# Performance work log

Measured on AMD Instinct MI355X. Metric: run time of the kernel, lower is better.

Reference implementation:

```python
import jax, jax.numpy as jnp
import numpy as np
import math

B, S, K, H, NH = 4, 1024, 512, 1024, 16
HD = H // NH  # 64


def _split_heads(x):
    # [B, L, H] -> [B, NH, L, HD]
    b, l, _ = x.shape
    return x.reshape(b, l, NH, HD).transpose(0, 2, 1, 3)


def setup_inputs() -> dict:
    key = jax.random.key(0)
    ks = jax.random.split(key, 16)
    scale = 1.0 / math.sqrt(H)
    d = {
        'hidden_states': jax.random.normal(ks[0], (B, S, H), jnp.float32),
        'encoder_hidden_states': jax.random.normal(ks[1], (B, K, H), jnp.float32),
        'attention_mask': jnp.zeros((B, 1, 1, S), jnp.float32),
        'encoder_attention_mask': jnp.zeros((B, 1, 1, K), jnp.float32),
    }
    names = ['q', 'k', 'v', 'kq', 'kk', 'kv']
    for i, n in enumerate(names):
        d[f'W{n}'] = jax.random.normal(ks[2 + i], (H, H), jnp.float32) * scale
        d[f'b{n}'] = jnp.zeros((H,), jnp.float32)
    return d


def reference(hidden_states, encoder_hidden_states, attention_mask, encoder_attention_mask,
              Wq, bq, Wk, bk, Wv, bv, Wkq, bkq, Wkk, bkk, Wkv, bkv):
    inv = 1.0 / math.sqrt(HD)
    # self branch
    q = _split_heads(hidden_states @ Wq + bq)            # [B,NH,S,HD]
    k = _split_heads(hidden_states @ Wk + bk)
    v = _split_heads(hidden_states @ Wv + bv)
    scores = jnp.einsum('bhsd,bhtd->bhst', q, k) * inv + attention_mask
    probs = jax.nn.softmax(scores, axis=-1)              # [B,NH,S,S]
    ctx = jnp.einsum('bhst,bhtd->bhsd', probs, v)
    # knowledge branch
    kq = _split_heads(hidden_states @ Wkq + bkq)          # [B,NH,S,HD]
    kk = _split_heads(encoder_hidden_states @ Wkk + bkk)  # [B,NH,K,HD]
    kv = _split_heads(encoder_hidden_states @ Wkv + bkv)
    kscores = jnp.einsum('bhsd,bhtd->bhst', kq, kk) * inv + encoder_attention_mask
    kprobs = jax.nn.softmax(kscores, axis=-1)            # [B,NH,S,K]
    kctx = jnp.einsum('bhst,bhtd->bhsd', kprobs, kv)
    # merge heads and average branches
    out = (ctx + kctx) * 0.5                             # [B,NH,S,HD]
    out = out.transpose(0, 2, 1, 3).reshape(B, S, H)
    return out
```

## Files before the change

kernel.cpp:

```cpp
#include <hip/hip_runtime.h>

#define BATCH 4
#define SEQ   1024
#define KENC  512
#define HDIM  1024
#define NHEAD 16
#define HD    64
#define LOG2E 1.44269504088896340736f

typedef __attribute__((ext_vector_type(8))) short bf16x8;
typedef __attribute__((ext_vector_type(4))) float f32x4;
typedef __attribute__((ext_vector_type(16))) float f32x16;
typedef __attribute__((ext_vector_type(4))) float f4v;
typedef __attribute__((ext_vector_type(4))) short s4v;

__device__ __forceinline__ short f2bf(float f) {
  unsigned u = __float_as_uint(f);
  u += 0x7fffu + ((u >> 16) & 1u);
  return (short)(u >> 16);
}

__device__ __forceinline__ void gload_lds16(const void* g, void* l) {
  __builtin_amdgcn_global_load_lds(
      (const __attribute__((address_space(1))) void*)g,
      (__attribute__((address_space(3))) void*)l, 16, 0, 0);
}

__global__ __launch_bounds__(256) void cast_bf16(const float* __restrict__ src,
                                                 short* __restrict__ dst, int n4) {
  int i = blockIdx.x * 256 + threadIdx.x;
  if (i >= n4) return;
  f4v v = ((const f4v*)src)[i];
  s4v o;
#pragma unroll
  for (int j = 0; j < 4; ++j) o[j] = f2bf(v[j]);
  ((s4v*)dst)[i] = o;
}

struct WtArgs { const float* W[6]; };

__global__ __launch_bounds__(256) void wt_cast(WtArgs a, short* __restrict__ wt) {
  int j = blockIdx.z;
  const float* W = a.W[j];
  short* dst = wt + (size_t)j * (HDIM * HDIM);
  int cb = blockIdx.x * 32, rb = blockIdx.y * 32;
  __shared__ float t[32][33];
  int tx = threadIdx.x & 31, ty = threadIdx.x >> 5;
#pragma unroll
  for (int rr = 0; rr < 4; ++rr)
    t[ty + rr * 8][tx] = W[(size_t)(rb + ty + rr * 8) * HDIM + cb + tx];
  __syncthreads();
#pragma unroll
  for (int rr = 0; rr < 4; ++rr)
    dst[(size_t)(cb + ty + rr * 8) * HDIM + rb + tx] = f2bf(t[tx][ty + rr * 8]);
}

struct ProjArgs {
  const short* X[6];
  const short* Wt[6];
  const float* bias[6];
  short* out[6];
  int M[6];
  int tshift[6];
  int mode[6];
  float scale[6];
};

__global__ __launch_bounds__(256) void proj_gemm(ProjArgs a) {
  int job = blockIdx.z;
  int M = a.M[job];
  int by = blockIdx.y;
  if (by * 128 >= M) return;
  int bx = blockIdx.x;
  const short* X = a.X[job];
  const short* W = a.Wt[job];

  __shared__ short As[128 * 32];
  __shared__ short Bs[128 * 32];

  int tid = threadIdx.x, lane = tid & 63, wave = tid >> 6;
  int wr = wave >> 1, wc = wave & 1;
  int l15 = lane & 15, g4 = lane >> 4;

  f32x4 acc[4][4];
#pragma unroll
  for (int m = 0; m < 4; ++m)
#pragma unroll
    for (int n = 0; n < 4; ++n)
#pragma unroll
      for (int r = 0; r < 4; ++r) acc[m][n][r] = 0.0f;

  int arow = by * 128, brow = bx * 128;
  const int crow = lane >> 2;
  const int sgrp = (lane & 3) ^ ((lane >> 2) & 3) ^ (lane >> 4);
  const int rsw = (lane & 3) ^ ((l15) >> 2);

  for (int k0 = 0; k0 < HDIM; k0 += 32) {
#pragma unroll
    for (int cc = 0; cc < 2; ++cc) {
      int c = wave * 2 + cc;
      gload_lds16(X + (size_t)(arow + c * 16 + crow) * HDIM + k0 + sgrp * 8,
                  (char*)As + c * 1024);
      gload_lds16(W + (size_t)(brow + c * 16 + crow) * HDIM + k0 + sgrp * 8,
                  (char*)Bs + c * 1024);
    }
    __syncthreads();
    bf16x8 af[4], bfr[4];
#pragma unroll
    for (int m = 0; m < 4; ++m)
      af[m] = *(const bf16x8*)((const char*)As + (wr * 64 + m * 16 + l15) * 64 +
                               ((g4 ^ rsw) << 4));
#pragma unroll
    for (int n = 0; n < 4; ++n)
      bfr[n] = *(const bf16x8*)((const char*)Bs + (wc * 64 + n * 16 + l15) * 64 +
                                ((g4 ^ rsw) << 4));
#pragma unroll
    for (int m = 0; m < 4; ++m)
#pragma unroll
      for (int n = 0; n < 4; ++n)
        acc[m][n] = __builtin_amdgcn_mfma_f32_16x16x32_bf16(af[m], bfr[n],
                                                            acc[m][n], 0, 0, 0);
    __syncthreads();
  }

  const float* bias = a.bias[job];
  short* out = a.out[job];
  int tshift = a.tshift[job], tmask = (1 << tshift) - 1, mode = a.mode[job];
  float scl = a.scale[job];
#pragma unroll
  for (int m = 0; m < 4; ++m) {
    int rowb = arow + wr * 64 + m * 16 + (g4 << 2);
#pragma unroll
    for (int n = 0; n < 4; ++n) {
      int col = brow + wc * 64 + n * 16 + l15;
      float bv = bias[col];
      int head = col >> 6, d = col & 63;
#pragma unroll
      for (int r = 0; r < 4; ++r) {
        int row = rowb + r;
        int bb = row >> tshift, t = row & tmask;
        float val = (acc[m][n][r] + bv) * scl;
        size_t idx;
        if (mode == 0)
          idx = ((((size_t)bb * NHEAD + head) << tshift) + t) * 64 + d;
        else
          idx = ((((size_t)bb * NHEAD + head) * 64 + d) << tshift) + t;
        out[idx] = f2bf(val);
      }
    }
  }
}

__global__ __launch_bounds__(256, 3) void attn32(
    const short* __restrict__ qall, const short* __restrict__ kall,
    const short* __restrict__ vTall, const short* __restrict__ kqall,
    const short* __restrict__ kkall, const short* __restrict__ kvTall,
    const float* __restrict__ amask, const float* __restrict__ emask,
    float* __restrict__ out) {
  __shared__ char KT[2][8192];
  __shared__ char VT[2][8192];
  __shared__ float red[4][32];

  int lid = blockIdx.x;
  int id = (lid & 7) * 64 + (lid >> 3);
  int bh = id >> 3, qb = id & 7;
  int b = bh >> 4, h = bh & 15;
  int lane = threadIdx.x & 63, wave = threadIdx.x >> 6;
  int l31 = lane & 31, hi = lane >> 5, x7 = l31 & 7;
  int qrow0 = qb * 128 + wave * 32;

  bf16x8 qcur[4];
  {
    const short* qp = qall + ((size_t)bh * SEQ + qrow0 + l31) * 64;
#pragma unroll
    for (int i = 0; i < 4; ++i)
      qcur[i] = *(const bf16x8*)(qp + i * 16 + hi * 8);
  }

  const char* kb0 = (const char*)(kall + (size_t)bh * SEQ * 64);
  const char* vb0 = (const char*)(vTall + (size_t)bh * 64 * SEQ);
  const char* kb1 = (const char*)(kkall + (size_t)bh * KENC * 64);
  const char* vb1 = (const char*)(kvTall + (size_t)bh * 64 * KENC);
  const float* mpc = amask + (size_t)b * SEQ;

  auto STAGE = [&](int pb, const char* kb, const char* vb, size_t vrowb, int kt) {
    int t0 = threadIdx.x;
#pragma unroll
    for (int c = 0; c < 2; ++c) {
      int idx = c * 256 + t0;
      int row = idx >> 3, phys = idx & 7;
      int lg = phys ^ (row & 7);
      gload_lds16(kb + ((size_t)(kt * 64 + row)) * 128 + lg * 16,
                  KT[pb] + idx * 16);
      gload_lds16(vb + (size_t)row * vrowb + (size_t)kt * 128 + lg * 16,
                  VT[pb] + idx * 16);
    }
  };

  STAGE(0, kb0, vb0, SEQ * 2, 0);

  f32x16 ctx0, ctx1, c10, c11;
#pragma unroll
  for (int r = 0; r < 16; ++r) { ctx0[r] = 0.f; ctx1[r] = 0.f; c10[r] = 0.f; c11[r] = 0.f; }
  float mr = -1e30f, lr = 0.f;

#pragma unroll 1
  for (int t = 0; t < 24; ++t) {
    int p = t & 1;
    __syncthreads();
    if (t < 23) {
      int tn = t + 1;
      if (tn >= 16) STAGE(p ^ 1, kb1, vb1, KENC * 2, tn - 16);
      else          STAGE(p ^ 1, kb0, vb0, SEQ * 2, tn);
    }
    if (t == 16) {
      if (!hi) red[wave][l31] = lr;
      asm volatile("s_waitcnt lgkmcnt(0)" ::: "memory");
#pragma unroll
      for (int r2 = 0; r2 < 4; ++r2) {
        f4v lv = *(const f4v*)(&red[wave][r2 * 8 + 4 * hi]);
#pragma unroll
        for (int j2 = 0; j2 < 4; ++j2) {
          float li = __builtin_amdgcn_rcpf(lv[j2]);
          int r = r2 * 4 + j2;
          c10[r] = ctx0[r] * li;  ctx0[r] = 0.f;
          c11[r] = ctx1[r] * li;  ctx1[r] = 0.f;
        }
      }
      mr = -1e30f; lr = 0.f;
      const short* kqp = kqall + ((size_t)bh * SEQ + qrow0 + l31) * 64;
#pragma unroll
      for (int i = 0; i < 4; ++i)
        qcur[i] = *(const bf16x8*)(kqp + i * 16 + hi * 8);
      mpc = emask + (size_t)b * KENC;
    }
    int kt = (t >= 16) ? t - 16 : t;
    const char* Kp = KT[p];
    const char* Vp = VT[p];

    f32x16 s0, s1;
#pragma unroll
    for (int r = 0; r < 16; ++r) { s0[r] = 0.f; s1[r] = 0.f; }
    __builtin_amdgcn_s_setprio(1);
#pragma unroll
    for (int i = 0; i < 4; ++i) {
      bf16x8 kf = *(const bf16x8*)(Kp + (l31)*128 + (((2 * i + hi) ^ x7) << 4));
      s0 = __builtin_amdgcn_mfma_f32_32x32x16_bf16(kf, qcur[i], s0, 0, 0, 0);
    }
#pragma unroll
    for (int i = 0; i < 4; ++i) {
      bf16x8 kf = *(const bf16x8*)(Kp + (32 + l31) * 128 + (((2 * i + hi) ^ x7) << 4));
      s1 = __builtin_amdgcn_mfma_f32_32x32x16_bf16(kf, qcur[i], s1, 0, 0, 0);
    }
    __builtin_amdgcn_s_setprio(0);

    const float* mp = mpc + kt * 64;
#pragma unroll
    for (int r2 = 0; r2 < 4; ++r2) {
      f4v ma = *(const f4v*)(mp + r2 * 8 + 4 * hi);
      f4v mb = *(const f4v*)(mp + 32 + r2 * 8 + 4 * hi);
#pragma unroll
      for (int j2 = 0; j2 < 4; ++j2) {
        s0[r2 * 4 + j2] = fmaf(ma[j2], LOG2E, s0[r2 * 4 + j2]);
        s1[r2 * 4 + j2] = fmaf(mb[j2], LOG2E, s1[r2 * 4 + j2]);
      }
    }

    float mx = s0[0];
#pragma unroll
    for (int r = 1; r < 16; ++r) mx = fmaxf(mx, s0[r]);
#pragma unroll
    for (int r = 0; r < 16; ++r) mx = fmaxf(mx, s1[r]);
    mx = fmaxf(mx, __int_as_float(__shfl_xor(__float_as_int(mx), 32)));

    if (!__all(mx <= mr + 12.f)) {
      float mn = fmaxf(mr, mx);
      float scl = __builtin_amdgcn_exp2f(mr - mn);
      mr = mn; lr *= scl;
      if (!hi) red[wave][l31] = scl;
      asm volatile("s_waitcnt lgkmcnt(0)" ::: "memory");
#pragma unroll
      for (int r2 = 0; r2 < 4; ++r2) {
        f4v sv = *(const f4v*)(&red[wave][r2 * 8 + 4 * hi]);
#pragma unroll
        for (int j2 = 0; j2 < 4; ++j2) {
          ctx0[r2 * 4 + j2] *= sv[j2];
          ctx1[r2 * 4 + j2] *= sv[j2];
        }
      }
    }

    float rs = 0.f;
#pragma unroll
    for (int r = 0; r < 16; ++r) { s0[r] = __builtin_amdgcn_exp2f(s0[r] - mr); rs += s0[r]; }
#pragma unroll
    for (int r = 0; r < 16; ++r) { s1[r] = __builtin_amdgcn_exp2f(s1[r] - mr); rs += s1[r]; }
    rs += __int_as_float(__shfl_xor(__float_as_int(rs), 32));
    lr += rs;

#pragma unroll
    for (int s = 0; s < 2; ++s) {
      const f32x16& sv = s ? s1 : s0;
      unsigned W[8];
#pragma unroll
      for (int r2 = 0; r2 < 4; ++r2) {
        asm("v_cvt_pk_bf16_f32 %0, %1, %2"
            : "=v"(W[r2 * 2]) : "v"(sv[r2 * 4 + 0]), "v"(sv[r2 * 4 + 1]));
        asm("v_cvt_pk_bf16_f32 %0, %1, %2"
            : "=v"(W[r2 * 2 + 1]) : "v"(sv[r2 * 4 + 2]), "v"(sv[r2 * 4 + 3]));
      }
#pragma unroll
      for (int jr = 0; jr < 2; ++jr) {
        unsigned sendA = hi ? W[(2 * jr) * 2]     : W[(2 * jr + 1) * 2];
        unsigned sendB = hi ? W[(2 * jr) * 2 + 1] : W[(2 * jr + 1) * 2 + 1];
        unsigned rA = (unsigned)__shfl_xor((int)sendA, 32);
        unsigned rB = (unsigned)__shfl_xor((int)sendB, 32);
        union { unsigned u[4]; bf16x8 v; } pa;
        if (!hi) { pa.u[0] = W[2 * jr * 2]; pa.u[1] = W[2 * jr * 2 + 1];
                   pa.u[2] = rA;            pa.u[3] = rB; }
        else     { pa.u[0] = rA;            pa.u[1] = rB;
                   pa.u[2] = W[(2 * jr + 1) * 2]; pa.u[3] = W[(2 * jr + 1) * 2 + 1]; }
        int j = s * 2 + jr;
        __builtin_amdgcn_s_setprio(1);
        bf16x8 vf0 = *(const bf16x8*)(Vp + (l31)*128 + (((2 * j + hi) ^ x7) << 4));
        ctx0 = __builtin_amdgcn_mfma_f32_32x32x16_bf16(pa.v, vf0, ctx0, 0, 0, 0);
        bf16x8 vf1 = *(const bf16x8*)(Vp + (32 + l31) * 128 + (((2 * j + hi) ^ x7) << 4));
        ctx1 = __builtin_amdgcn_mfma_f32_32x32x16_bf16(pa.v, vf1, ctx1, 0, 0, 0);
        __builtin_amdgcn_s_setprio(0);
      }
    }
  }

  if (!hi) red[wave][l31] = lr;
  asm volatile("s_waitcnt lgkmcnt(0)" ::: "memory");
  float* op = out + ((size_t)b * SEQ) * HDIM + h * 64 + l31;
#pragma unroll
  for (int r2 = 0; r2 < 4; ++r2) {
    f4v lv = *(const f4v*)(&red[wave][r2 * 8 + 4 * hi]);
#pragma unroll
    for (int j2 = 0; j2 < 4; ++j2) {
      float li = __builtin_amdgcn_rcpf(lv[j2]);
      int s = qrow0 + r2 * 8 + 4 * hi + j2;
      int r = r2 * 4 + j2;
      op[(size_t)s * HDIM]      = 0.5f * (c10[r] + ctx0[r] * li);
      op[(size_t)s * HDIM + 32] = 0.5f * (c11[r] + ctx1[r] * li);
    }
  }
}

extern "C" void kernel_launch(void* const* d_in, const int* in_sizes, int n_in,
                              void* d_out, int out_size, void* d_ws, size_t ws_size,
                              hipStream_t stream) {
  const float* hid = (const float*)d_in[0];
  const float* enc = (const float*)d_in[1];
  const float* amask = (const float*)d_in[2];
  const float* emask = (const float*)d_in[3];

  char* ws = (char*)d_ws;
  short* hbf = (short*)(ws);
  short* ebf = (short*)(ws + (8u << 20));
  short* wt = (short*)(ws + (12u << 20));
  short* qo = (short*)(ws + (24u << 20));
  short* ko = (short*)(ws + (32u << 20));
  short* vT = (short*)(ws + (40u << 20));
  short* kqo = (short*)(ws + (48u << 20));
  short* kko = (short*)(ws + (56u << 20));
  short* kvT = (short*)(ws + (60u << 20));

  cast_bf16<<<4096, 256, 0, stream>>>(hid, hbf, (BATCH * SEQ * HDIM) / 4);
  cast_bf16<<<2048, 256, 0, stream>>>(enc, ebf, (BATCH * KENC * HDIM) / 4);

  WtArgs wa;
  for (int j = 0; j < 6; ++j) wa.W[j] = (const float*)d_in[4 + 2 * j];
  wt_cast<<<dim3(32, 32, 6), 256, 0, stream>>>(wa, wt);

  ProjArgs pa;
  const short* Xs[6] = {hbf, hbf, hbf, hbf, ebf, ebf};
  short* outs[6] = {qo, ko, vT, kqo, kko, kvT};
  const int Ms[6] = {4096, 4096, 4096, 4096, 2048, 2048};
  const int tsh[6] = {10, 10, 10, 10, 9, 9};
  const int md[6] = {0, 0, 1, 0, 0, 1};
  const float qscale = 0.125f * LOG2E;
  const float scl[6] = {qscale, 1.f, 1.f, qscale, 1.f, 1.f};
  for (int j = 0; j < 6; ++j) {
    pa.X[j] = Xs[j];
    pa.Wt[j] = wt + (size_t)j * (HDIM * HDIM);
    pa.bias[j] = (const float*)d_in[5 + 2 * j];
    pa.out[j] = outs[j];
    pa.M[j] = Ms[j];
    pa.tshift[j] = tsh[j];
    pa.mode[j] = md[j];
    pa.scale[j] = scl[j];
  }
  proj_gemm<<<dim3(8, 32, 6), 256, 0, stream>>>(pa);

  attn32<<<512, 256, 0, stream>>>(qo, ko, vT, kqo, kko, kvT, amask, emask,
                                  (float*)d_out);
}
```

Measured before the change: 147.6 us.

## Pipeline projection GEMM with four-stage LDS ring buffer and async prefetch

Replaces the single-buffered load/sync/compute loop in the projection GEMM with a four-buffer LDS ring. Three K-tiles are prefetched ahead with direct global-to-LDS loads, and partial vmcnt waits let global loads overlap the MFMA work. Wave priority is raised around the MFMA block. The cost is 64KB of LDS per block, which can lower occupancy, and more complex hand-managed waits and barriers.

```diff
diff --git a/kernel.cpp b/kernel.cpp
--- a/kernel.cpp
+++ b/kernel.cpp
@@ -75,8 +75,7 @@
   const short* X = a.X[job];
   const short* W = a.Wt[job];
 
-  __shared__ short As[128 * 32];
-  __shared__ short Bs[128 * 32];
+  __shared__ __align__(16) char Lds[4][16384];
 
   int tid = threadIdx.x, lane = tid & 63, wave = tid >> 6;
   int wr = wave >> 1, wc = wave & 1;
@@ -93,35 +92,73 @@
   int arow = by * 128, brow = bx * 128;
   const int crow = lane >> 2;
   const int sgrp = (lane & 3) ^ ((lane >> 2) & 3) ^ (lane >> 4);
-  const int rsw = (lane & 3) ^ ((l15) >> 2);
-
-  for (int k0 = 0; k0 < HDIM; k0 += 32) {
-#pragma unroll
-    for (int cc = 0; cc < 2; ++cc) {
-      int c = wave * 2 + cc;
-      gload_lds16(X + (size_t)(arow + c * 16 + crow) * HDIM + k0 + sgrp * 8,
-                  (char*)As + c * 1024);
-      gload_lds16(W + (size_t)(brow + c * 16 + crow) * HDIM + k0 + sgrp * 8,
-                  (char*)Bs + c * 1024);
-    }
-    __syncthreads();
-    bf16x8 af[4], bfr[4];
-#pragma unroll
-    for (int m = 0; m < 4; ++m)
-      af[m] = *(const bf16x8*)((const char*)As + (wr * 64 + m * 16 + l15) * 64 +
-                               ((g4 ^ rsw) << 4));
-#pragma unroll
-    for (int n = 0; n < 4; ++n)
-      bfr[n] = *(const bf16x8*)((const char*)Bs + (wc * 64 + n * 16 + l15) * 64 +
-                                ((g4 ^ rsw) << 4));
-#pragma unroll
-    for (int m = 0; m < 4; ++m)
-#pragma unroll
-      for (int n = 0; n < 4; ++n)
-        acc[m][n] = __builtin_amdgcn_mfma_f32_16x16x32_bf16(af[m], bfr[n],
-                                                            acc[m][n], 0, 0, 0);
-    __syncthreads();
-  }
+  const int rsw = (lane & 3) ^ (l15 >> 2);
+
+  const short* Xb = X + (size_t)arow * HDIM + (size_t)crow * HDIM + sgrp * 8;
+  const short* Wb = W + (size_t)brow * HDIM + (size_t)crow * HDIM + sgrp * 8;
+
+#define STAGE(buf, kt)                                                        \
+  do {                                                                        \
+    _Pragma("unroll") for (int cc = 0; cc < 2; ++cc) {                        \
+      int c = wave * 2 + cc;                                                  \
+      gload_lds16(Xb + (size_t)c * 16 * HDIM + (kt) * 32,                     \
+                  (char*)Lds[buf] + c * 1024 + lane * 16);                    \
+      gload_lds16(Wb + (size_t)c * 16 * HDIM + (kt) * 32,                     \
+                  (char*)Lds[buf] + 8192 + c * 1024 + lane * 16);             \
+    }                                                                         \
+  } while (0)
+
+
+  int aoff = (wr * 64 + l15) * 64 + ((g4 ^ rsw) << 4);
+  int boff = 8192 + (wc * 64 + l15) * 64 + ((g4 ^ rsw) << 4);
+
+  STAGE(0, 0);
+  STAGE(1, 1);
+  STAGE(2, 2);
+  asm volatile("s_waitcnt vmcnt(8)" ::: "memory");
+  __builtin_amdgcn_s_barrier();
+  asm volatile("" ::: "memory");
+
+  bf16x8 af[4], bfr[4];
+
+#define STEP(BUF, DO_STG, SBUF, SKT, WAITN, DO_BAR)                           \
+  do {                                                                        \
+    _Pragma("unroll") for (int m = 0; m < 4; ++m)                             \
+        af[m] = *(const bf16x8*)((const char*)Lds[BUF] + m * 1024 + aoff);    \
+    _Pragma("unroll") for (int n = 0; n < 4; ++n)                             \
+        bfr[n] = *(const bf16x8*)((const char*)Lds[BUF] + n * 1024 + boff);   \
+    if (DO_STG) STAGE(SBUF, SKT);                                             \
+    __builtin_amdgcn_s_setprio(1);                                            \
+    _Pragma("unroll") for (int m = 0; m < 4; ++m)                             \
+        _Pragma("unroll") for (int n = 0; n < 4; ++n)                         \
+            acc[m][n] = __builtin_amdgcn_mfma_f32_16x16x32_bf16(              \
+                af[m], bfr[n], acc[m][n], 0, 0, 0);                           \
+    __builtin_amdgcn_s_setprio(0);                                            \
+    if (WAITN >= 0) {                                                         \
+      if (WAITN == 8) asm volatile("s_waitcnt vmcnt(8)" ::: "memory");        \
+      else if (WAITN == 4) asm volatile("s_waitcnt vmcnt(4)" ::: "memory");   \
+      else asm volatile("s_waitcnt vmcnt(0)" ::: "memory");                   \
+    }                                                                         \
+    if (DO_BAR) {                                                             \
+      __builtin_amdgcn_s_barrier();                                           \
+      asm volatile("" ::: "memory");                                          \
+    }                                                                         \
+  } while (0)
+
+#pragma unroll 1
+  for (int t = 0; t < 28; t += 4) {
+    STEP(0, 1, 3, t + 3, 8, 1);
+    STEP(1, 1, 0, t + 4, 8, 1);
+    STEP(2, 1, 1, t + 5, 8, 1);
+    STEP(3, 1, 2, t + 6, 8, 1);
+  }
+  STEP(0, 1, 3, 31, 8, 1);
+  STEP(1, 0, 0, 0, 4, 1);
+  STEP(2, 0, 0, 0, 0, 1);
+  STEP(3, 0, 0, 0, -1, 0);
+
+#undef STEP
+#undef STAGE
 
   const float* bias = a.bias[job];
   short* out = a.out[job];
```

Result: no change. 147.4 us (-0.1%).

## Software-pipeline projection GEMM with 4-stage LDS ring and register double-buffering

Applied to the files above, without the earlier changes.

Rewrites the projection GEMM main loop to use a four-stage LDS ring buffer filled by asynchronous global-to-LDS loads issued three k-steps ahead. Fragment reads for the next step are double-buffered in registers and interleaved with MFMA groups, and s_setprio raises priority around the MFMA bursts. This aims to hide global load latency and remove one of the two barriers per k-step. The cost is 64KB of LDS per block, which reduces occupancy, plus fragile manual vmcnt accounting.

```diff
diff --git a/kernel.cpp b/kernel.cpp
--- a/kernel.cpp
+++ b/kernel.cpp
@@ -25,6 +25,8 @@
       (const __attribute__((address_space(1))) void*)g,
       (__attribute__((address_space(3))) void*)l, 16, 0, 0);
 }
+
+#define MF(A, B, C) __builtin_amdgcn_mfma_f32_16x16x32_bf16((A), (B), (C), 0, 0, 0)
 
 __global__ __launch_bounds__(256) void cast_bf16(const float* __restrict__ src,
                                                  short* __restrict__ dst, int n4) {
@@ -75,8 +77,7 @@
   const short* X = a.X[job];
   const short* W = a.Wt[job];
 
-  __shared__ short As[128 * 32];
-  __shared__ short Bs[128 * 32];
+  __shared__ __align__(16) char Lds[65536];
 
   int tid = threadIdx.x, lane = tid & 63, wave = tid >> 6;
   int wr = wave >> 1, wc = wave & 1;
@@ -93,35 +94,113 @@
   int arow = by * 128, brow = bx * 128;
   const int crow = lane >> 2;
   const int sgrp = (lane & 3) ^ ((lane >> 2) & 3) ^ (lane >> 4);
-  const int rsw = (lane & 3) ^ ((l15) >> 2);
-
-  for (int k0 = 0; k0 < HDIM; k0 += 32) {
-#pragma unroll
-    for (int cc = 0; cc < 2; ++cc) {
-      int c = wave * 2 + cc;
-      gload_lds16(X + (size_t)(arow + c * 16 + crow) * HDIM + k0 + sgrp * 8,
-                  (char*)As + c * 1024);
-      gload_lds16(W + (size_t)(brow + c * 16 + crow) * HDIM + k0 + sgrp * 8,
-                  (char*)Bs + c * 1024);
-    }
-    __syncthreads();
-    bf16x8 af[4], bfr[4];
-#pragma unroll
-    for (int m = 0; m < 4; ++m)
-      af[m] = *(const bf16x8*)((const char*)As + (wr * 64 + m * 16 + l15) * 64 +
-                               ((g4 ^ rsw) << 4));
-#pragma unroll
-    for (int n = 0; n < 4; ++n)
-      bfr[n] = *(const bf16x8*)((const char*)Bs + (wc * 64 + n * 16 + l15) * 64 +
-                                ((g4 ^ rsw) << 4));
-#pragma unroll
-    for (int m = 0; m < 4; ++m)
-#pragma unroll
-      for (int n = 0; n < 4; ++n)
-        acc[m][n] = __builtin_amdgcn_mfma_f32_16x16x32_bf16(af[m], bfr[n],
-                                                            acc[m][n], 0, 0, 0);
-    __syncthreads();
-  }
+  const int rsw = (lane & 3) ^ (l15 >> 2);
+
+  const char* Xb = (const char*)X;
+  const char* Wb = (const char*)W;
+  const size_t sac0 = ((size_t)(arow + 32 * wave + crow) * HDIM + sgrp * 8) * 2;
+  const size_t sac1 = sac0 + (size_t)16 * HDIM * 2;
+  const size_t sbc0 = ((size_t)(brow + 32 * wave + crow) * HDIM + sgrp * 8) * 2;
+  const size_t sbc1 = sbc0 + (size_t)16 * HDIM * 2;
+  const int ldA0 = wave * 2048, ldA1 = ldA0 + 1024;
+  const int ldB0 = 8192 + ldA0, ldB1 = ldB0 + 1024;
+
+  const int aoff = wr * 4096 + l15 * 64 + ((g4 ^ rsw) << 4);
+  const int boff = 8192 + wc * 4096 + l15 * 64 + ((g4 ^ rsw) << 4);
+
+#define STG_A(SBO, SKT)                                                  \
+  do {                                                                   \
+    gload_lds16(Xb + sac0 + (size_t)(SKT) * 64, Lds + (SBO) + ldA0);     \
+    gload_lds16(Xb + sac1 + (size_t)(SKT) * 64, Lds + (SBO) + ldA1);     \
+  } while (0)
+#define STG_B(SBO, SKT)                                                  \
+  do {                                                                   \
+    gload_lds16(Wb + sbc0 + (size_t)(SKT) * 64, Lds + (SBO) + ldB0);     \
+    gload_lds16(Wb + sbc1 + (size_t)(SKT) * 64, Lds + (SBO) + ldB1);     \
+  } while (0)
+
+  STG_A(0, 0);     STG_B(0, 0);
+  STG_A(16384, 1); STG_B(16384, 1);
+  STG_A(32768, 2); STG_B(32768, 2);
+  asm volatile("s_waitcnt vmcnt(4)" ::: "memory");
+  __builtin_amdgcn_s_barrier();
+  asm volatile("" ::: "memory");
+
+  bf16x8 xa0, xa1, xb0, xb1, xb2, xb3;
+  bf16x8 ya0, ya1, yb0, yb1, yb2, yb3;
+
+  xa0 = *(const bf16x8*)(Lds + 0 * 1024 + aoff);
+  xa1 = *(const bf16x8*)(Lds + 1 * 1024 + aoff);
+  xb0 = *(const bf16x8*)(Lds + 0 * 1024 + boff);
+  xb1 = *(const bf16x8*)(Lds + 1 * 1024 + boff);
+  xb2 = *(const bf16x8*)(Lds + 2 * 1024 + boff);
+  xb3 = *(const bf16x8*)(Lds + 3 * 1024 + boff);
+
+#define GSTEP_I(BO, BON, CA0, CA1, CB0, CB1, CB2, CB3, NA0, NA1, NB0, NB1,    \
+                NB2, NB3, DO_STG, SBO, SKT, DO_NEXT, VMASM, DO_BAR)           \
+  do {                                                                        \
+    bf16x8 q2 = *(const bf16x8*)(Lds + (BO) + 2 * 1024 + aoff);               \
+    bf16x8 q3 = *(const bf16x8*)(Lds + (BO) + 3 * 1024 + aoff);               \
+    if (DO_STG) STG_A(SBO, SKT);                                              \
+    __builtin_amdgcn_s_setprio(1);                                            \
+    acc[0][0] = MF(CA0, CB0, acc[0][0]);                                      \
+    acc[0][1] = MF(CA0, CB1, acc[0][1]);                                      \
+    acc[0][2] = MF(CA0, CB2, acc[0][2]);                                      \
+    acc[0][3] = MF(CA0, CB3, acc[0][3]);                                      \
+    acc[1][0] = MF(CA1, CB0, acc[1][0]);                                      \
+    acc[1][1] = MF(CA1, CB1, acc[1][1]);                                      \
+    acc[1][2] = MF(CA1, CB2, acc[1][2]);                                      \
+    acc[1][3] = MF(CA1, CB3, acc[1][3]);                                      \
+    __builtin_amdgcn_s_setprio(0);                                            \
+    if (DO_NEXT) {                                                            \
+      NA0 = *(const bf16x8*)(Lds + (BON) + 0 * 1024 + aoff);                  \
+      NA1 = *(const bf16x8*)(Lds + (BON) + 1 * 1024 + aoff);                  \
+      NB0 = *(const bf16x8*)(Lds + (BON) + 0 * 1024 + boff);                  \
+      NB1 = *(const bf16x8*)(Lds + (BON) + 1 * 1024 + boff);                  \
+      NB2 = *(const bf16x8*)(Lds + (BON) + 2 * 1024 + boff);                  \
+      NB3 = *(const bf16x8*)(Lds + (BON) + 3 * 1024 + boff);                  \
+    }                                                                         \
+    if (DO_STG) STG_B(SBO, SKT);                                              \
+    __builtin_amdgcn_s_setprio(1);                                            \
+    acc[2][0] = MF(q2, CB0, acc[2][0]);                                       \
+    acc[2][1] = MF(q2, CB1, acc[2][1]);                                       \
+    acc[2][2] = MF(q2, CB2, acc[2][2]);                                       \
+    acc[2][3] = MF(q2, CB3, acc[2][3]);                                       \
+    acc[3][0] = MF(q3, CB0, acc[3][0]);                                       \
+    acc[3][1] = MF(q3, CB1, acc[3][1]);                                       \
+    acc[3][2] = MF(q3, CB2, acc[3][2]);                                       \
+    acc[3][3] = MF(q3, CB3, acc[3][3]);                                       \
+    __builtin_amdgcn_s_setprio(0);                                            \
+    asm volatile(VMASM ::: "memory");                                         \
+    if (DO_BAR) {                                                             \
+      __builtin_amdgcn_s_barrier();                                           \
+      asm volatile("" ::: "memory");                                          \
+    }                                                                         \
+  } while (0)
+#define GSTEP(...) GSTEP_I(__VA_ARGS__)
+
+#define XSET xa0, xa1, xb0, xb1, xb2, xb3
+#define YSET ya0, ya1, yb0, yb1, yb2, yb3
+
+#pragma unroll 1
+  for (int it = 0; it < 7; ++it) {
+    int t0 = it * 4;
+    GSTEP(0,     16384, XSET, YSET, 1, 49152, t0 + 3, 1, "s_waitcnt vmcnt(4)", 1);
+    GSTEP(16384, 32768, YSET, XSET, 1, 0,     t0 + 4, 1, "s_waitcnt vmcnt(4)", 1);
+    GSTEP(32768, 49152, XSET, YSET, 1, 16384, t0 + 5, 1, "s_waitcnt vmcnt(4)", 1);
+    GSTEP(49152, 0,     YSET, XSET, 1, 32768, t0 + 6, 1, "s_waitcnt vmcnt(4)", 1);
+  }
+  GSTEP(0,     16384, XSET, YSET, 1, 49152, 31, 1, "s_waitcnt vmcnt(4)", 1);
+  GSTEP(16384, 32768, YSET, XSET, 0, 0, 0,      1, "s_waitcnt vmcnt(0)", 1);
+  GSTEP(32768, 49152, XSET, YSET, 0, 0, 0,      1, "s_nop 0", 1);
+  GSTEP(49152, 0,     YSET, XSET, 0, 0, 0,      0, "s_nop 0", 0);
+
+#undef GSTEP
+#undef GSTEP_I
+#undef XSET
+#undef YSET
+#undef STG_A
+#undef STG_B
 
   const float* bias = a.bias[job];
   short* out = a.out[job];
```

Measured after the change: 146.6 us. About the same (-0.7%).
